# Optimization experiments

Hardware: AMD Instinct MI355X
Metric: run time of the kernel (lower is better)

Reference implementation:

```python
import jax, jax.numpy as jnp
from jax import lax
import numpy as np
import math

D = 96   # d_model
H = 4    # num_heads (d_k = d_v = D per head, per the source)
K = 7    # depthwise kernel size
L = 4    # num conv layers


def _pos_encoding(seq_len, d):
    # Faithful to the source's (nonstandard) exponents: sin uses 2*i/d, cos uses 2*(i+1)/d
    pos = np.arange(seq_len, dtype=np.float32)[:, None]
    i = np.arange(0, d, 2, dtype=np.float32)
    pe = np.zeros((seq_len, d), dtype=np.float32)
    pe[:, 0::2] = np.sin(pos / 10000.0 ** (2.0 * i / d))
    pe[:, 1::2] = np.cos(pos / 10000.0 ** (2.0 * (i + 1.0) / d))
    return jnp.asarray(pe)


def _layernorm(x, g, b, eps=1e-5):
    m = jnp.mean(x, axis=-1, keepdims=True)
    v = jnp.mean((x - m) ** 2, axis=-1, keepdims=True)
    return (x - m) / jnp.sqrt(v + eps) * g + b


def setup_inputs() -> dict:
    key = jax.random.key(0)
    ks = jax.random.split(key, 10)
    B, S = 128, 384

    def xavier(k, shape, fan_in, fan_out):
        bound = math.sqrt(6.0 / (fan_in + fan_out))
        return jax.random.uniform(k, shape, jnp.float32, -bound, bound)

    return {
        "input": jax.random.normal(ks[0], (B, S, D), jnp.float32),
        "mask": jnp.zeros((B, S), dtype=bool),
        "conv_dw": jax.random.normal(ks[1], (L, D, 1, K), jnp.float32) * 0.05,
        "conv_dw_b": jnp.zeros((L, D), jnp.float32),
        "conv_pw": jax.random.normal(ks[2], (L, D, D, 1), jnp.float32) * 0.05,
        "conv_pw_b": jnp.zeros((L, D), jnp.float32),
        "WQ": xavier(ks[3], (H, D, D), D, D),
        "WK": xavier(ks[4], (H, D, D), D, D),
        "WV": xavier(ks[5], (H, D, D), D, D),
        "WO": xavier(ks[6], (H * D, D), H * D, D),
        "ffn_w1": jax.random.normal(ks[7], (D, D // 2), jnp.float32) * 0.1,
        "ffn_b1": jnp.zeros((D // 2,), jnp.float32),
        "ffn_w2": jax.random.normal(ks[8], (D // 2, D), jnp.float32) * 0.1,
        "ffn_b2": jnp.zeros((D,), jnp.float32),
        "ln_g": jnp.ones((L + 2, D), jnp.float32),
        "ln_b": jnp.zeros((L + 2, D), jnp.float32),
    }


def reference(input, mask, conv_dw, conv_dw_b, conv_pw, conv_pw_b,
              WQ, WK, WV, WO, ffn_w1, ffn_b1, ffn_w2, ffn_b2, ln_g, ln_b):
    B, S, _ = input.shape
    dn = ("NCH", "OIH", "NCH")

    # positional encoding (eval mode: all dropout is identity)
    x = input * jnp.float32(math.sqrt(D)) + _pos_encoding(S, D)[None]

    # conv blocks: LN -> depthwise conv -> pointwise conv -> relu -> residual
    for i in range(L):
        h = _layernorm(x, ln_g[i], ln_b[i])
        h = jnp.transpose(h, (0, 2, 1))  # [B, C, S]
        h = lax.conv_general_dilated(h, conv_dw[i], (1,), "SAME",
                                     feature_group_count=D, dimension_numbers=dn)
        h = h + conv_dw_b[i][None, :, None]
        h = lax.conv_general_dilated(h, conv_pw[i], (1,), "SAME", dimension_numbers=dn)
        h = jax.nn.relu(h + conv_pw_b[i][None, :, None])
        x = x + jnp.transpose(h, (0, 2, 1))

    # multi-head attention with per-head full-width projections (d_k = D)
    h = _layernorm(x, ln_g[L], ln_b[L])
    Q = jnp.einsum("bsd,hde->hbse", h, WQ)
    Kh = jnp.einsum("bsd,hde->hbse", h, WK)
    V = jnp.einsum("bsd,hde->hbse", h, WV)
    # source divides scores by temperature = 1/sqrt(d_k) => multiply by sqrt(D)
    scores = jnp.einsum("hbqe,hbke->hbqk", Q, Kh) * jnp.float32(math.sqrt(D))
    # mask is viewed [B, S, 1]: masks query rows, broadcast over keys
    scores = jnp.where(mask[None, :, :, None], -jnp.inf, scores)
    attn = jax.nn.softmax(scores, axis=-1)
    ctx = jnp.einsum("hbqk,hbke->hbqe", attn, V)
    cat = jnp.transpose(ctx, (1, 2, 0, 3)).reshape(B, S, H * D)
    x = x + cat @ WO

    # feed-forward: Linear -> sigmoid -> Linear, residual
    h2 = _layernorm(x, ln_g[L + 1], ln_b[L + 1])
    ff = jax.nn.sigmoid(h2 @ ffn_w1 + ffn_b1) @ ffn_w2 + ffn_b2
    return x + ff
```

## Files before the change

kernel.cpp:

```cpp
#include <hip/hip_runtime.h>
#include <math.h>


constexpr int B = 128;
constexpr int S = 384;
constexpr int D = 96;
constexpr int H = 4;
constexpr int KW = 7;
constexpr int L = 4;
constexpr int ROWS = B * S;
constexpr long long NTOT = (long long)ROWS * D;
constexpr float SQRTD = 9.797958971132712f;

typedef _Float16 f16x8 __attribute__((ext_vector_type(8)));
typedef float f32x4 __attribute__((ext_vector_type(4)));
typedef unsigned short us;
typedef unsigned short us8 __attribute__((ext_vector_type(8)));

__device__ __forceinline__ us f2h(float f) {
    _Float16 h = (_Float16)f;
    return __builtin_bit_cast(us, h);
}
__device__ __forceinline__ f16x8 ldh(const us* p) {
    return *reinterpret_cast<const f16x8*>(p);
}

__global__ void pe_kernel(float* __restrict__ pe) {
    int idx = blockIdx.x * 256 + threadIdx.x;
    if (idx >= S * D) return;
    int s = idx / D, c = idx - s * D;
    int j = c >> 1;
    float expo = (c & 1) ? (4.0f * j + 2.0f) / 96.0f : (4.0f * j) / 96.0f;
    float freq = expf(-expo * logf(10000.0f));
    float ang = (float)s * freq;
    pe[idx] = (c & 1) ? cosf(ang) : sinf(ang);
}

__global__ void prep_w(const float* __restrict__ WQ, const float* __restrict__ WK,
                       const float* __restrict__ cpw, const float* __restrict__ w1,
                       const float* __restrict__ w2,
                       us* __restrict__ wqS, us* __restrict__ wkT, us* __restrict__ pw16,
                       us* __restrict__ w1T, us* __restrict__ w2Tp) {
    int idx = blockIdx.x * 256 + threadIdx.x;
    if (idx >= H * D * D) return;
    int h = idx / (D * D), rem = idx - h * (D * D);
    int d = rem / D, e = rem - d * D;
    int n = e >> 4, lmod = e & 15, kk = d >> 5, ldiv = (d >> 3) & 3, j = d & 7;
    wqS[(size_t)(((h * 6 + n) * 3 + kk) * 64 + ldiv * 16 + lmod) * 8 + j] = f2h(WQ[idx] * SQRTD);
    wkT[(size_t)h * D * D + e * D + d] = f2h(WK[idx]);
    pw16[idx] = f2h(cpw[idx]);
    if (idx < 48 * 96) {
        int m = idx / 96, c = idx - m * 96;
        w1T[idx] = f2h(w1[c * 48 + m]);
    }
    if (idx < 96 * 64) {
        int o = idx / 64, m = idx - o * 64;
        w2Tp[idx] = (m < 48) ? f2h(w2[m * 96 + o]) : (us)0;
    }
}

__global__ void prep_wvo(const float* __restrict__ WV, const float* __restrict__ WO,
                         us* __restrict__ wvoT) {
    int blk = blockIdx.x;
    int h = blk / 6, ot = blk - h * 6;
    int tid = threadIdx.x;
    const float* wv = WV + (size_t)h * D * D;
    const float* wo = WO + (size_t)h * D * D;
    for (int i = tid; i < 16 * 96; i += 256) {
        int o = ot * 16 + i / 96, d = i - (i / 96) * 96;
        float acc = 0.f;
        for (int e = 0; e < 96; e++) acc += wv[d * 96 + e] * wo[e * 96 + o];
        wvoT[(size_t)h * D * D + o * 96 + d] = f2h(acc);
    }
}

__global__ void conv0f(const float* __restrict__ in, const float* __restrict__ pe,
                       const float* __restrict__ g0, const float* __restrict__ b0,
                       float* __restrict__ xout, us* __restrict__ lnout,
                       const float* __restrict__ dwW, const float* __restrict__ dwB,
                       const us* __restrict__ pwW, const float* __restrict__ pwb,
                       const float* __restrict__ gnext, const float* __restrict__ bnext) {
    __shared__ us lnb_s[70 * 104];
    __shared__ us dwb_s[64 * 104];
    __shared__ float lw[96 * 8];
    int tid = threadIdx.x;
    int wave = tid >> 6, lane = tid & 63;
    int r0 = blockIdx.x * 64;
    int b = r0 / S, s0 = r0 % S;

    for (int i = tid; i < 96 * KW; i += 256) lw[(i / KW) * 8 + (i % KW)] = dwW[i];

    for (int i = wave; i < 70; i += 4) {
        int s = s0 - 3 + i;
        bool valid = (unsigned)s < (unsigned)S;
        float v0 = 0.f, v1 = 0.f;
        if (valid) {
            size_t ro = ((size_t)b * S + s) * 96;
            v0 = in[ro + lane] * SQRTD + pe[s * 96 + lane];
            v1 = (lane < 32) ? in[ro + 64 + lane] * SQRTD + pe[s * 96 + 64 + lane] : 0.f;
        }
        float sm = v0 + v1, q = v0 * v0 + v1 * v1;
        for (int off = 32; off > 0; off >>= 1) {
            sm += __shfl_xor(sm, off);
            q += __shfl_xor(q, off);
        }
        float mean = sm * (1.0f / D);
        float var = q * (1.0f / D) - mean * mean;
        float rstd = rsqrtf(var + 1e-5f);
        lnb_s[i * 104 + lane] = f2h(valid ? (v0 - mean) * rstd * g0[lane] + b0[lane] : 0.f);
        if (lane < 32)
            lnb_s[i * 104 + 64 + lane] =
                f2h(valid ? (v1 - mean) * rstd * g0[lane + 64] + b0[lane + 64] : 0.f);
    }
    __syncthreads();

    for (int u = tid; u < 768; u += 256) {
        int j = u / 12, c0 = (u - (u / 12) * 12) * 8;
        float acc[8];
        #pragma unroll
        for (int j2 = 0; j2 < 8; j2++) acc[j2] = dwB[c0 + j2];
        #pragma unroll
        for (int k = 0; k < KW; k++) {
            f16x8 v = ldh(&lnb_s[(j + k) * 104 + c0]);
            #pragma unroll
            for (int j2 = 0; j2 < 8; j2++) acc[j2] += (float)v[j2] * lw[(c0 + j2) * 8 + k];
        }
        us8 o;
        #pragma unroll
        for (int j2 = 0; j2 < 8; j2++) o[j2] = f2h(acc[j2]);
        *reinterpret_cast<us8*>(&dwb_s[j * 104 + c0]) = o;
    }
    __syncthreads();

    int lmod = lane & 15, ldiv = lane >> 4, m0 = wave * 16;
    f32x4 acc[6] = {};
    #pragma unroll
    for (int kk = 0; kk < 3; kk++) {
        f16x8 af = ldh(&dwb_s[(m0 + lmod) * 104 + kk * 32 + ldiv * 8]);
        #pragma unroll
        for (int n = 0; n < 6; n++) {
            f16x8 bf = ldh(pwW + (size_t)(n * 16 + lmod) * 96 + kk * 32 + ldiv * 8);
            acc[n] = __builtin_amdgcn_mfma_f32_16x16x32_f16(af, bf, acc[n], 0, 0, 0);
        }
    }

    float gv[6], bv2[6], pb[6];
    #pragma unroll
    for (int n = 0; n < 6; n++) {
        int o = n * 16 + lmod;
        gv[n] = gnext[o];
        bv2[n] = bnext[o];
        pb[n] = pwb[o];
    }
    #pragma unroll
    for (int n = 0; n < 6; n++) {
        int o = n * 16 + lmod;
        #pragma unroll
        for (int r = 0; r < 4; r++) {
            int sr = m0 + ldiv * 4 + r;
            size_t row = (size_t)r0 + sr;
            float base = in[row * 96 + o] * SQRTD + pe[(s0 + sr) * 96 + o];
            acc[n][r] = base + fmaxf(acc[n][r] + pb[n], 0.f);
        }
    }
    #pragma unroll
    for (int r = 0; r < 4; r++) {
        float sm = 0.f, qq = 0.f;
        #pragma unroll
        for (int n = 0; n < 6; n++) {
            sm += acc[n][r];
            qq += acc[n][r] * acc[n][r];
        }
        #pragma unroll
        for (int st = 1; st <= 8; st <<= 1) {
            sm += __shfl_xor(sm, st);
            qq += __shfl_xor(qq, st);
        }
        float mean = sm * (1.0f / D);
        float var = qq * (1.0f / D) - mean * mean;
        float rstd = rsqrtf(var + 1e-5f);
        size_t row = (size_t)r0 + m0 + ldiv * 4 + r;
        #pragma unroll
        for (int n = 0; n < 6; n++) {
            int o = n * 16 + lmod;
            xout[row * 96 + o] = acc[n][r];
            lnout[row * 96 + o] = f2h((acc[n][r] - mean) * rstd * gv[n] + bv2[n]);
        }
    }
}

__global__ void conv2(const float* __restrict__ xin, const us* __restrict__ lnin,
                      float* __restrict__ xout, us* __restrict__ lnout,
                      const float* __restrict__ dwW, const float* __restrict__ dwB,
                      const us* __restrict__ pwW, const float* __restrict__ pwb,
                      const float* __restrict__ gnext, const float* __restrict__ bnext) {
    __shared__ us dwb_s[64 * 104];
    __shared__ float lw[96 * 8];
    int tid = threadIdx.x;
    int wave = tid >> 6, lane = tid & 63;
    int r0 = blockIdx.x * 64;
    int b = r0 / S, s0 = r0 % S;

    for (int i = tid; i < 96 * KW; i += 256) lw[(i / KW) * 8 + (i % KW)] = dwW[i];
    __syncthreads();

    for (int u = tid; u < 768; u += 256) {
        int j = u / 12, c0 = (u - (u / 12) * 12) * 8;
        float acc[8];
        #pragma unroll
        for (int j2 = 0; j2 < 8; j2++) acc[j2] = dwB[c0 + j2];
        #pragma unroll
        for (int k = 0; k < KW; k++) {
            int ss = s0 + j + k - 3;
            if ((unsigned)ss < (unsigned)S) {
                f16x8 v = ldh(lnin + ((size_t)b * S + ss) * 96 + c0);
                #pragma unroll
                for (int j2 = 0; j2 < 8; j2++) acc[j2] += (float)v[j2] * lw[(c0 + j2) * 8 + k];
            }
        }
        us8 o;
        #pragma unroll
        for (int j2 = 0; j2 < 8; j2++) o[j2] = f2h(acc[j2]);
        *reinterpret_cast<us8*>(&dwb_s[j * 104 + c0]) = o;
    }
    __syncthreads();

    int lmod = lane & 15, ldiv = lane >> 4, m0 = wave * 16;
    f32x4 acc[6] = {};
    #pragma unroll
    for (int kk = 0; kk < 3; kk++) {
        f16x8 af = ldh(&dwb_s[(m0 + lmod) * 104 + kk * 32 + ldiv * 8]);
        #pragma unroll
        for (int n = 0; n < 6; n++) {
            f16x8 bf = ldh(pwW + (size_t)(n * 16 + lmod) * 96 + kk * 32 + ldiv * 8);
            acc[n] = __builtin_amdgcn_mfma_f32_16x16x32_f16(af, bf, acc[n], 0, 0, 0);
        }
    }

    float gv[6], bv2[6], pb[6];
    #pragma unroll
    for (int n = 0; n < 6; n++) {
        int o = n * 16 + lmod;
        gv[n] = gnext[o];
        bv2[n] = bnext[o];
        pb[n] = pwb[o];
    }
    #pragma unroll
    for (int n = 0; n < 6; n++) {
        #pragma unroll
        for (int r = 0; r < 4; r++) {
            size_t row = (size_t)r0 + m0 + ldiv * 4 + r;
            acc[n][r] = xin[row * 96 + n * 16 + lmod] + fmaxf(acc[n][r] + pb[n], 0.f);
        }
    }
    #pragma unroll
    for (int r = 0; r < 4; r++) {
        float sm = 0.f, qq = 0.f;
        #pragma unroll
        for (int n = 0; n < 6; n++) {
            sm += acc[n][r];
            qq += acc[n][r] * acc[n][r];
        }
        #pragma unroll
        for (int st = 1; st <= 8; st <<= 1) {
            sm += __shfl_xor(sm, st);
            qq += __shfl_xor(qq, st);
        }
        float mean = sm * (1.0f / D);
        float var = qq * (1.0f / D) - mean * mean;
        float rstd = rsqrtf(var + 1e-5f);
        size_t row = (size_t)r0 + m0 + ldiv * 4 + r;
        #pragma unroll
        for (int n = 0; n < 6; n++) {
            int o = n * 16 + lmod;
            xout[row * 96 + o] = acc[n][r];
            lnout[row * 96 + o] = f2h((acc[n][r] - mean) * rstd * gv[n] + bv2[n]);
        }
    }
}

__global__ void conv3p(const float* __restrict__ xin, const us* __restrict__ lnin,
                       float* __restrict__ xout, us* __restrict__ lnout,
                       const float* __restrict__ dwW, const float* __restrict__ dwB,
                       const us* __restrict__ pwW, const float* __restrict__ pwb,
                       const float* __restrict__ gnext, const float* __restrict__ bnext,
                       const us* __restrict__ wkT, const us* __restrict__ wvoT,
                       us* __restrict__ Kall, us* __restrict__ Vall) {
    __shared__ float lw[96 * 8];
    __shared__ us stg[96 * 72];
    __shared__ us lnstg[64 * 104];
    int tid = threadIdx.x;
    int wave = tid >> 6, lane = tid & 63;
    int lmod = lane & 15, ldiv = lane >> 4, m0 = wave * 16;
    int r0 = blockIdx.x * 64;
    int b = r0 / S, s0 = r0 % S;

    for (int i = tid; i < 96 * KW; i += 256) lw[(i / KW) * 8 + (i % KW)] = dwW[i];
    __syncthreads();

    for (int u = tid; u < 768; u += 256) {
        int j = u / 12, c0 = (u - (u / 12) * 12) * 8;
        float acc[8];
        #pragma unroll
        for (int j2 = 0; j2 < 8; j2++) acc[j2] = dwB[c0 + j2];
        #pragma unroll
        for (int k = 0; k < KW; k++) {
            int ss = s0 + j + k - 3;
            if ((unsigned)ss < (unsigned)S) {
                f16x8 v = ldh(lnin + ((size_t)b * S + ss) * 96 + c0);
                #pragma unroll
                for (int j2 = 0; j2 < 8; j2++) acc[j2] += (float)v[j2] * lw[(c0 + j2) * 8 + k];
            }
        }
        us8 o;
        #pragma unroll
        for (int j2 = 0; j2 < 8; j2++) o[j2] = f2h(acc[j2]);
        *reinterpret_cast<us8*>(&stg[j * 104 + c0]) = o;
    }
    __syncthreads();

    f32x4 acc[6] = {};
    #pragma unroll
    for (int kk = 0; kk < 3; kk++) {
        f16x8 af = ldh(&stg[(m0 + lmod) * 104 + kk * 32 + ldiv * 8]);
        #pragma unroll
        for (int n = 0; n < 6; n++) {
            f16x8 bf = ldh(pwW + (size_t)(n * 16 + lmod) * 96 + kk * 32 + ldiv * 8);
            acc[n] = __builtin_amdgcn_mfma_f32_16x16x32_f16(af, bf, acc[n], 0, 0, 0);
        }
    }

    float gv[6], bv2[6], pb[6];
    #pragma unroll
    for (int n = 0; n < 6; n++) {
        int o = n * 16 + lmod;
        gv[n] = gnext[o];
        bv2[n] = bnext[o];
        pb[n] = pwb[o];
    }
    #pragma unroll
    for (int n = 0; n < 6; n++) {
        #pragma unroll
        for (int r = 0; r < 4; r++) {
            size_t row = (size_t)r0 + m0 + ldiv * 4 + r;
            acc[n][r] = xin[row * 96 + n * 16 + lmod] + fmaxf(acc[n][r] + pb[n], 0.f);
        }
    }
    #pragma unroll
    for (int r = 0; r < 4; r++) {
        float sm = 0.f, qq = 0.f;
        #pragma unroll
        for (int n = 0; n < 6; n++) {
            sm += acc[n][r];
            qq += acc[n][r] * acc[n][r];
        }
        #pragma unroll
        for (int st = 1; st <= 8; st <<= 1) {
            sm += __shfl_xor(sm, st);
            qq += __shfl_xor(qq, st);
        }
        float mean = sm * (1.0f / D);
        float var = qq * (1.0f / D) - mean * mean;
        float rstd = rsqrtf(var + 1e-5f);
        size_t row = (size_t)r0 + m0 + ldiv * 4 + r;
        #pragma unroll
        for (int n = 0; n < 6; n++) {
            int o = n * 16 + lmod;
            xout[row * 96 + o] = acc[n][r];
            us hv = f2h((acc[n][r] - mean) * rstd * gv[n] + bv2[n]);
            lnout[row * 96 + o] = hv;
            lnstg[(m0 + ldiv * 4 + r) * 104 + o] = hv;
        }
    }
    __syncthreads();

    f16x8 af[3];
    #pragma unroll
    for (int kk = 0; kk < 3; kk++)
        af[kk] = ldh(&lnstg[(m0 + lmod) * 104 + kk * 32 + ldiv * 8]);

    for (int hd = 0; hd < H; hd++) {
        f32x4 ka[6] = {};
        #pragma unroll
        for (int kk = 0; kk < 3; kk++)
            #pragma unroll
            for (int n = 0; n < 6; n++) {
                f16x8 bf =
                    ldh(wkT + (size_t)hd * D * D + (size_t)(n * 16 + lmod) * 96 + kk * 32 + ldiv * 8);
                ka[n] = __builtin_amdgcn_mfma_f32_16x16x32_f16(af[kk], bf, ka[n], 0, 0, 0);
            }
        __syncthreads();
        us* kT = stg + wave * 1664;
        #pragma unroll
        for (int n = 0; n < 6; n++)
            #pragma unroll
            for (int r = 0; r < 4; r++)
                kT[(ldiv * 4 + r) * 104 + n * 16 + lmod] = f2h(ka[n][r]);
        int t0 = (r0 % S) / 16 + wave;
        us* dst = Kall + (size_t)hd * NTOT + ((size_t)(b * 24 + t0) * 3) * 512;
        #pragma unroll
        for (int kk = 0; kk < 3; kk++) {
            us8 v = *reinterpret_cast<const us8*>(&kT[lmod * 104 + kk * 32 + ldiv * 8]);
            *reinterpret_cast<us8*>(dst + kk * 512 + lane * 8) = v;
        }
        f32x4 va[6] = {};
        #pragma unroll
        for (int kk = 0; kk < 3; kk++)
            #pragma unroll
            for (int n = 0; n < 6; n++) {
                f16x8 bf = ldh(wvoT + (size_t)hd * D * D + (size_t)(n * 16 + lmod) * 96 + kk * 32 +
                               ldiv * 8);
                va[n] = __builtin_amdgcn_mfma_f32_16x16x32_f16(af[kk], bf, va[n], 0, 0, 0);
            }
        __syncthreads();
        #pragma unroll
        for (int n = 0; n < 6; n++)
            #pragma unroll
            for (int r = 0; r < 4; r++)
                stg[(n * 16 + lmod) * 72 + m0 + ldiv * 4 + r] = f2h(va[n][r]);
        __syncthreads();
        int cblk = (r0 % S) / 64;
        us* dsth = Vall + (size_t)hd * NTOT;
        #pragma unroll
        for (int n = 0; n < 6; n++)
            #pragma unroll
            for (int kk = 0; kk < 2; kk++) {
                us8 v =
                    *reinterpret_cast<const us8*>(&stg[(n * 16 + lmod) * 72 + kk * 32 + ldiv * 8]);
                *reinterpret_cast<us8*>(
                    dsth + ((size_t)((b * 6 + n) * 6 + cblk) * 2 + kk) * 512 + lane * 8) = v;
            }
    }
}

__global__ __launch_bounds__(256, 2) void attn_2p4(const us* __restrict__ h16,
                                                   const us* __restrict__ wqS,
                                                   const us* __restrict__ Kall,
                                                   const us* __restrict__ Vall,
                                                   us* __restrict__ xpart) {
    __shared__ us stg4[4][32 * 104];
    int tid = threadIdx.x, wave = tid >> 6, lane = tid & 63;
    us* stg = stg4[wave];
    int lmod = lane & 15, ldiv = lane >> 4;
    int p = blockIdx.x;
    int gl = (((p & 7) * 192 + (p >> 3)) << 2) + wave;
    int t = gl % 12;
    int bh = gl / 12;
    int b = bh >> 2, hd = bh & 3;
    size_t rowbase = (size_t)b * S + t * 32;

    f16x8 ah0[3], ah1[3];
    #pragma unroll
    for (int kk = 0; kk < 3; kk++) {
        ah0[kk] = ldh(h16 + (rowbase + lmod) * 96 + kk * 32 + ldiv * 8);
        ah1[kk] = ldh(h16 + (rowbase + 16 + lmod) * 96 + kk * 32 + ldiv * 8);
    }

    f32x4 qa0[6] = {}, qa1[6] = {};
    #pragma unroll
    for (int kk = 0; kk < 3; kk++)
        #pragma unroll
        for (int n = 0; n < 6; n++) {
            f16x8 bf = ldh(wqS + (size_t)(((hd * 6 + n) * 3 + kk) * 64) * 8 + lane * 8);
            qa0[n] = __builtin_amdgcn_mfma_f32_16x16x32_f16(ah0[kk], bf, qa0[n], 0, 0, 0);
            qa1[n] = __builtin_amdgcn_mfma_f32_16x16x32_f16(ah1[kk], bf, qa1[n], 0, 0, 0);
        }
    #pragma unroll
    for (int n = 0; n < 6; n++)
        #pragma unroll
        for (int r = 0; r < 4; r++) {
            stg[(ldiv * 4 + r) * 104 + n * 16 + lmod] = f2h(qa0[n][r]);
            stg[(16 + ldiv * 4 + r) * 104 + n * 16 + lmod] = f2h(qa1[n][r]);
        }
    f16x8 aq0[3], aq1[3];
    #pragma unroll
    for (int kk = 0; kk < 3; kk++) {
        aq0[kk] = ldh(&stg[lmod * 104 + kk * 32 + ldiv * 8]);
        aq1[kk] = ldh(&stg[(16 + lmod) * 104 + kk * 32 + ldiv * 8]);
    }

    const us* Kh = Kall + (size_t)hd * NTOT + (size_t)b * 24 * 1536;
    const us* Vh = Vall + (size_t)hd * NTOT + (size_t)b * 36 * 1024;

    f32x4 mx0 = {-1e30f, -1e30f, -1e30f, -1e30f}, mx1 = mx0;
    for (int c = 0; c < 6; c++) {
        f32x4 s0[4] = {}, s1[4] = {};
        __builtin_amdgcn_s_setprio(1);
        #pragma unroll
        for (int nt = 0; nt < 4; nt++)
            #pragma unroll
            for (int kk = 0; kk < 3; kk++) {
                f16x8 bf = ldh(Kh + (size_t)((c * 4 + nt) * 3 + kk) * 512 + lane * 8);
                s0[nt] = __builtin_amdgcn_mfma_f32_16x16x32_f16(aq0[kk], bf, s0[nt], 0, 0, 0);
                s1[nt] = __builtin_amdgcn_mfma_f32_16x16x32_f16(aq1[kk], bf, s1[nt], 0, 0, 0);
            }
        __builtin_amdgcn_s_setprio(0);
        #pragma unroll
        for (int nt = 0; nt < 4; nt++)
            #pragma unroll
            for (int r = 0; r < 4; r++) {
                mx0[r] = fmaxf(mx0[r], s0[nt][r]);
                mx1[r] = fmaxf(mx1[r], s1[nt][r]);
            }
    }
    #pragma unroll
    for (int st = 1; st <= 8; st <<= 1)
        #pragma unroll
        for (int r = 0; r < 4; r++) {
            mx0[r] = fmaxf(mx0[r], __shfl_xor(mx0[r], st));
            mx1[r] = fmaxf(mx1[r], __shfl_xor(mx1[r], st));
        }

    f32x4 oacc0[6] = {}, oacc1[6] = {};
    f32x4 l0v = {}, l1v = {};
    for (int c = 0; c < 6; c++) {
        f32x4 s0[4] = {}, s1[4] = {};
        __builtin_amdgcn_s_setprio(1);
        #pragma unroll
        for (int nt = 0; nt < 4; nt++)
            #pragma unroll
            for (int kk = 0; kk < 3; kk++) {
                f16x8 bf = ldh(Kh + (size_t)((c * 4 + nt) * 3 + kk) * 512 + lane * 8);
                s0[nt] = __builtin_amdgcn_mfma_f32_16x16x32_f16(aq0[kk], bf, s0[nt], 0, 0, 0);
                s1[nt] = __builtin_amdgcn_mfma_f32_16x16x32_f16(aq1[kk], bf, s1[nt], 0, 0, 0);
            }
        __builtin_amdgcn_s_setprio(0);
        #pragma unroll
        for (int nt = 0; nt < 4; nt++)
            #pragma unroll
            for (int r = 0; r < 4; r++) {
                float p0 = __expf(s0[nt][r] - mx0[r]);
                float p1 = __expf(s1[nt][r] - mx1[r]);
                l0v[r] += p0;
                l1v[r] += p1;
                stg[(ldiv * 4 + r) * 72 + nt * 16 + lmod] = f2h(p0);
                stg[(16 + ldiv * 4 + r) * 72 + nt * 16 + lmod] = f2h(p1);
            }
        __builtin_amdgcn_s_setprio(1);
        #pragma unroll
        for (int kk = 0; kk < 2; kk++) {
            f16x8 pf0 = ldh(&stg[lmod * 72 + kk * 32 + ldiv * 8]);
            f16x8 pf1 = ldh(&stg[(16 + lmod) * 72 + kk * 32 + ldiv * 8]);
            #pragma unroll
            for (int n = 0; n < 6; n++) {
                f16x8 bf = ldh(Vh + (size_t)((n * 6 + c) * 2 + kk) * 512 + lane * 8);
                oacc0[n] = __builtin_amdgcn_mfma_f32_16x16x32_f16(pf0, bf, oacc0[n], 0, 0, 0);
                oacc1[n] = __builtin_amdgcn_mfma_f32_16x16x32_f16(pf1, bf, oacc1[n], 0, 0, 0);
            }
        }
        __builtin_amdgcn_s_setprio(0);
    }
    #pragma unroll
    for (int st = 1; st <= 8; st <<= 1)
        #pragma unroll
        for (int r = 0; r < 4; r++) {
            l0v[r] += __shfl_xor(l0v[r], st);
            l1v[r] += __shfl_xor(l1v[r], st);
        }

    us* xp = xpart + (size_t)hd * NTOT;
    #pragma unroll
    for (int r = 0; r < 4; r++) {
        float inv0 = 1.f / l0v[r];
        float inv1 = 1.f / l1v[r];
        #pragma unroll
        for (int n = 0; n < 6; n++) {
            xp[(rowbase + ldiv * 4 + r) * 96 + n * 16 + lmod] = f2h(oacc0[n][r] * inv0);
            xp[(rowbase + 16 + ldiv * 4 + r) * 96 + n * 16 + lmod] = f2h(oacc1[n][r] * inv1);
        }
    }
}

__global__ void ffn_ln(const float* __restrict__ x, const us* __restrict__ xpart,
                       const float* __restrict__ gln, const float* __restrict__ bln,
                       const us* __restrict__ w1T, const float* __restrict__ b1,
                       const us* __restrict__ w2Tp, const float* __restrict__ b2,
                       float* __restrict__ out) {
    __shared__ float xf[64 * 96];
    __shared__ us lnb[64 * 104];
    __shared__ us mid[64 * 72];
    int tid = threadIdx.x, wave = tid >> 6, lane = tid & 63;
    int lmod = lane & 15, ldiv = lane >> 4, m0 = wave * 16;
    int row0 = blockIdx.x * 64;

    for (int i = wave; i < 64; i += 4) {
        size_t ro = (size_t)(row0 + i) * 96;
        float v0 = x[ro + lane];
        float v1 = (lane < 32) ? x[ro + 64 + lane] : 0.f;
        #pragma unroll
        for (int h = 0; h < H; h++) {
            const us* xp = xpart + (size_t)h * NTOT + ro;
            v0 += (float)__builtin_bit_cast(_Float16, xp[lane]);
            if (lane < 32) v1 += (float)__builtin_bit_cast(_Float16, xp[64 + lane]);
        }
        xf[i * 96 + lane] = v0;
        if (lane < 32) xf[i * 96 + 64 + lane] = v1;
        float sm = v0 + v1, q = v0 * v0 + v1 * v1;
        for (int off = 32; off > 0; off >>= 1) {
            sm += __shfl_xor(sm, off);
            q += __shfl_xor(q, off);
        }
        float mean = sm * (1.0f / D);
        float var = q * (1.0f / D) - mean * mean;
        float rstd = rsqrtf(var + 1e-5f);
        lnb[i * 104 + lane] = f2h((v0 - mean) * rstd * gln[lane] + bln[lane]);
        if (lane < 32)
            lnb[i * 104 + 64 + lane] = f2h((v1 - mean) * rstd * gln[lane + 64] + bln[lane + 64]);
    }
    __syncthreads();

    f32x4 a3[3] = {};
    #pragma unroll
    for (int kk = 0; kk < 3; kk++) {
        f16x8 af = ldh(&lnb[(m0 + lmod) * 104 + kk * 32 + ldiv * 8]);
        #pragma unroll
        for (int n = 0; n < 3; n++) {
            f16x8 bf = ldh(w1T + (size_t)(n * 16 + lmod) * 96 + kk * 32 + ldiv * 8);
            a3[n] = __builtin_amdgcn_mfma_f32_16x16x32_f16(af, bf, a3[n], 0, 0, 0);
        }
    }
    #pragma unroll
    for (int n = 0; n < 3; n++) {
        float bv = b1[n * 16 + lmod];
        #pragma unroll
        for (int r = 0; r < 4; r++) {
            float v = a3[n][r] + bv;
            mid[(m0 + ldiv * 4 + r) * 72 + n * 16 + lmod] = f2h(1.f / (1.f + __expf(-v)));
        }
    }
    #pragma unroll
    for (int r = 0; r < 4; r++) mid[(m0 + ldiv * 4 + r) * 72 + 48 + lmod] = 0;
    __syncthreads();

    f32x4 a6[6] = {};
    #pragma unroll
    for (int kk = 0; kk < 2; kk++) {
        f16x8 af = ldh(&mid[(m0 + lmod) * 72 + kk * 32 + ldiv * 8]);
        #pragma unroll
        for (int n = 0; n < 6; n++) {
            f16x8 bf = ldh(w2Tp + (size_t)(n * 16 + lmod) * 64 + kk * 32 + ldiv * 8);
            a6[n] = __builtin_amdgcn_mfma_f32_16x16x32_f16(af, bf, a6[n], 0, 0, 0);
        }
    }
    #pragma unroll
    for (int n = 0; n < 6; n++) {
        int o = n * 16 + lmod;
        float bv = b2[o];
        #pragma unroll
        for (int r = 0; r < 4; r++) {
            int sr = m0 + ldiv * 4 + r;
            out[(size_t)(row0 + sr) * 96 + o] = xf[sr * 96 + o] + a6[n][r] + bv;
        }
    }
}

extern "C" void kernel_launch(void* const* d_in, const int* in_sizes, int n_in,
                              void* d_out, int out_size, void* d_ws, size_t ws_size,
                              hipStream_t stream) {
    const float* in   = (const float*)d_in[0];
    const float* cdw  = (const float*)d_in[2];
    const float* cdwb = (const float*)d_in[3];
    const float* cpw  = (const float*)d_in[4];
    const float* cpwb = (const float*)d_in[5];
    const float* WQ   = (const float*)d_in[6];
    const float* WK   = (const float*)d_in[7];
    const float* WV   = (const float*)d_in[8];
    const float* WO   = (const float*)d_in[9];
    const float* w1   = (const float*)d_in[10];
    const float* b1   = (const float*)d_in[11];
    const float* w2   = (const float*)d_in[12];
    const float* b2   = (const float*)d_in[13];
    const float* lng  = (const float*)d_in[14];
    const float* lnb  = (const float*)d_in[15];
    float* out = (float*)d_out;
    float* ws = (float*)d_ws;

    float* xA  = ws;
    float* xB  = xA + NTOT;
    float* pe  = xB + NTOT;
    us* lnA    = (us*)(pe + S * D);
    us* lnB    = lnA + NTOT;
    us* Kall   = lnB + NTOT;
    us* Vall   = Kall + (size_t)H * NTOT;
    us* xpart  = Vall + (size_t)H * NTOT;
    us* wqS    = xpart + (size_t)H * NTOT;
    us* wkT    = wqS + H * D * D;
    us* wvoT   = wkT + H * D * D;
    us* pw16   = wvoT + H * D * D;
    us* w1T    = pw16 + L * D * D;
    us* w2Tp   = w1T + 48 * 96;

    pe_kernel<<<(S * D + 255) / 256, 256, 0, stream>>>(pe);
    prep_w<<<(H * D * D + 255) / 256, 256, 0, stream>>>(WQ, WK, cpw, w1, w2,
                                                        wqS, wkT, pw16, w1T, w2Tp);
    prep_wvo<<<H * 6, 256, 0, stream>>>(WV, WO, wvoT);

    conv0f<<<ROWS / 64, 256, 0, stream>>>(in, pe, lng, lnb, xA, lnB,
                                          cdw, cdwb, pw16, cpwb, lng + D, lnb + D);
    conv2<<<ROWS / 64, 256, 0, stream>>>(xA, lnB, xB, lnA, cdw + D * KW, cdwb + D,
                                         pw16 + D * D, cpwb + D, lng + 2 * D, lnb + 2 * D);
    conv2<<<ROWS / 64, 256, 0, stream>>>(xB, lnA, xA, lnB, cdw + 2 * D * KW, cdwb + 2 * D,
                                         pw16 + 2 * D * D, cpwb + 2 * D, lng + 3 * D,
                                         lnb + 3 * D);
    conv3p<<<ROWS / 64, 256, 0, stream>>>(xA, lnB, xB, lnA, cdw + 3 * D * KW, cdwb + 3 * D,
                                          pw16 + 3 * D * D, cpwb + 3 * D, lng + 4 * D,
                                          lnb + 4 * D, wkT, wvoT, Kall, Vall);

    attn_2p4<<<1536, 256, 0, stream>>>(lnA, wqS, Kall, Vall, xpart);

    ffn_ln<<<ROWS / 64, 256, 0, stream>>>(xB, xpart, lng + 5 * D, lnb + 5 * D,
                                          w1T, b1, w2Tp, b2, out);
}
```

Baseline: 334.4 us.

## Software-pipeline attention second pass with double-buffered P tiles

Restructures the softmax/PV loop so the QK scores for chunk c+1 are computed before the PV MFMAs for chunk c, with the exponentiated probabilities written to alternating LDS buffers. The aim is to overlap score MFMAs and global K loads with PV work and the exp/store phase, hiding latency within each wave. It adds extra LDS per block (a second P buffer) and raises register pressure from holding two score sets live, which could cause spills under the two-blocks-per-CU launch bound.

Result: no change. 337.8 us (+1.0%).

```diff
diff --git a/kernel.cpp b/kernel.cpp
--- a/kernel.cpp
+++ b/kernel.cpp
@@ -433,14 +433,52 @@
     }
 }
 
+#define SCORE(CC, S0, S1)                                                                   \
+    __builtin_amdgcn_s_setprio(1);                                                          \
+    _Pragma("unroll") for (int nt = 0; nt < 4; nt++) {                                      \
+        _Pragma("unroll") for (int kk = 0; kk < 3; kk++) {                                  \
+            f16x8 bf = ldh(Kh + (size_t)(((CC) * 4 + nt) * 3 + kk) * 512 + lane * 8);       \
+            S0[nt] = __builtin_amdgcn_mfma_f32_16x16x32_f16(aq0[kk], bf, S0[nt], 0, 0, 0);  \
+            S1[nt] = __builtin_amdgcn_mfma_f32_16x16x32_f16(aq1[kk], bf, S1[nt], 0, 0, 0);  \
+        }                                                                                   \
+    }                                                                                       \
+    __builtin_amdgcn_s_setprio(0);
+
+#define EXPSTORE(S0, S1, BUF)                                      \
+    _Pragma("unroll") for (int nt = 0; nt < 4; nt++) {             \
+        _Pragma("unroll") for (int r = 0; r < 4; r++) {            \
+            float p0 = __expf(S0[nt][r] - mx0[r]);                 \
+            float p1 = __expf(S1[nt][r] - mx1[r]);                 \
+            l0v[r] += p0;                                          \
+            l1v[r] += p1;                                          \
+            (BUF)[(ldiv * 4 + r) * 72 + nt * 16 + lmod] = f2h(p0); \
+            (BUF)[(16 + ldiv * 4 + r) * 72 + nt * 16 + lmod] = f2h(p1); \
+        }                                                          \
+    }
+
+#define PVSTEP(CC, BUF)                                                                     \
+    __builtin_amdgcn_s_setprio(1);                                                          \
+    _Pragma("unroll") for (int kk = 0; kk < 2; kk++) {                                      \
+        f16x8 pf0 = ldh((BUF) + lmod * 72 + kk * 32 + ldiv * 8);                            \
+        f16x8 pf1 = ldh((BUF) + (16 + lmod) * 72 + kk * 32 + ldiv * 8);                     \
+        _Pragma("unroll") for (int n = 0; n < 6; n++) {                                     \
+            f16x8 bf = ldh(Vh + (size_t)((n * 6 + (CC)) * 2 + kk) * 512 + lane * 8);        \
+            oacc0[n] = __builtin_amdgcn_mfma_f32_16x16x32_f16(pf0, bf, oacc0[n], 0, 0, 0);  \
+            oacc1[n] = __builtin_amdgcn_mfma_f32_16x16x32_f16(pf1, bf, oacc1[n], 0, 0, 0);  \
+        }                                                                                   \
+    }                                                                                       \
+    __builtin_amdgcn_s_setprio(0);
+
 __global__ __launch_bounds__(256, 2) void attn_2p4(const us* __restrict__ h16,
                                                    const us* __restrict__ wqS,
                                                    const us* __restrict__ Kall,
                                                    const us* __restrict__ Vall,
                                                    us* __restrict__ xpart) {
     __shared__ us stg4[4][32 * 104];
+    __shared__ us stgP[4][32 * 72];
     int tid = threadIdx.x, wave = tid >> 6, lane = tid & 63;
     us* stg = stg4[wave];
+    us* bufB = stgP[wave];
     int lmod = lane & 15, ldiv = lane >> 4;
     int p = blockIdx.x;
     int gl = (((p & 7) * 192 + (p >> 3)) << 2) + wave;
@@ -485,16 +523,7 @@
     f32x4 mx0 = {-1e30f, -1e30f, -1e30f, -1e30f}, mx1 = mx0;
     for (int c = 0; c < 6; c++) {
         f32x4 s0[4] = {}, s1[4] = {};
-        __builtin_amdgcn_s_setprio(1);
-        #pragma unroll
-        for (int nt = 0; nt < 4; nt++)
-            #pragma unroll
-            for (int kk = 0; kk < 3; kk++) {
-                f16x8 bf = ldh(Kh + (size_t)((c * 4 + nt) * 3 + kk) * 512 + lane * 8);
-                s0[nt] = __builtin_amdgcn_mfma_f32_16x16x32_f16(aq0[kk], bf, s0[nt], 0, 0, 0);
-                s1[nt] = __builtin_amdgcn_mfma_f32_16x16x32_f16(aq1[kk], bf, s1[nt], 0, 0, 0);
-            }
-        __builtin_amdgcn_s_setprio(0);
+        SCORE(c, s0, s1)
         #pragma unroll
         for (int nt = 0; nt < 4; nt++)
             #pragma unroll
@@ -513,42 +542,22 @@
 
     f32x4 oacc0[6] = {}, oacc1[6] = {};
     f32x4 l0v = {}, l1v = {};
+    {
+        f32x4 s0[4] = {}, s1[4] = {};
+        SCORE(0, s0, s1)
+        EXPSTORE(s0, s1, stg)
+    }
     for (int c = 0; c < 6; c++) {
-        f32x4 s0[4] = {}, s1[4] = {};
-        __builtin_amdgcn_s_setprio(1);
-        #pragma unroll
-        for (int nt = 0; nt < 4; nt++)
-            #pragma unroll
-            for (int kk = 0; kk < 3; kk++) {
-                f16x8 bf = ldh(Kh + (size_t)((c * 4 + nt) * 3 + kk) * 512 + lane * 8);
-                s0[nt] = __builtin_amdgcn_mfma_f32_16x16x32_f16(aq0[kk], bf, s0[nt], 0, 0, 0);
-                s1[nt] = __builtin_amdgcn_mfma_f32_16x16x32_f16(aq1[kk], bf, s1[nt], 0, 0, 0);
-            }
-        __builtin_amdgcn_s_setprio(0);
-        #pragma unroll
-        for (int nt = 0; nt < 4; nt++)
-            #pragma unroll
-            for (int r = 0; r < 4; r++) {
-                float p0 = __expf(s0[nt][r] - mx0[r]);
-                float p1 = __expf(s1[nt][r] - mx1[r]);
-                l0v[r] += p0;
-                l1v[r] += p1;
-                stg[(ldiv * 4 + r) * 72 + nt * 16 + lmod] = f2h(p0);
-                stg[(16 + ldiv * 4 + r) * 72 + nt * 16 + lmod] = f2h(p1);
-            }
-        __builtin_amdgcn_s_setprio(1);
-        #pragma unroll
-        for (int kk = 0; kk < 2; kk++) {
-            f16x8 pf0 = ldh(&stg[lmod * 72 + kk * 32 + ldiv * 8]);
-            f16x8 pf1 = ldh(&stg[(16 + lmod) * 72 + kk * 32 + ldiv * 8]);
-            #pragma unroll
-            for (int n = 0; n < 6; n++) {
-                f16x8 bf = ldh(Vh + (size_t)((n * 6 + c) * 2 + kk) * 512 + lane * 8);
-                oacc0[n] = __builtin_amdgcn_mfma_f32_16x16x32_f16(pf0, bf, oacc0[n], 0, 0, 0);
-                oacc1[n] = __builtin_amdgcn_mfma_f32_16x16x32_f16(pf1, bf, oacc1[n], 0, 0, 0);
-            }
-        }
-        __builtin_amdgcn_s_setprio(0);
+        f32x4 t0[4] = {}, t1[4] = {};
+        if (c < 5) {
+            SCORE(c + 1, t0, t1)
+        }
+        us* rb = (c & 1) ? bufB : stg;
+        PVSTEP(c, rb)
+        if (c < 5) {
+            us* wb = (c & 1) ? stg : bufB;
+            EXPSTORE(t0, t1, wb)
+        }
     }
     #pragma unroll
     for (int st = 1; st <= 8; st <<= 1)
```

## Share K/V tiles across waves via double-buffered LDS in attention kernel

Applied to the files above, without the earlier changes.

The attention kernel is restructured so that each block's four waves handle 128 consecutive queries of the same batch/head and cooperatively stage K and V chunks into double-buffered shared memory. Previously each wave streamed K and V from global memory on its own. The V tensor layout written by the conv3p kernel is reordered so that each key chunk is contiguous. This cuts redundant global/L2 traffic for K/V, at the cost of block-wide barriers each chunk and roughly 75KB of LDS per block, which may limit the intended two blocks per CU.

Result: faster. 304.5 us (-8.9%).

```diff
diff --git a/kernel.cpp b/kernel.cpp
--- a/kernel.cpp
+++ b/kernel.cpp
@@ -428,69 +428,91 @@
                 us8 v =
                     *reinterpret_cast<const us8*>(&stg[(n * 16 + lmod) * 72 + kk * 32 + ldiv * 8]);
                 *reinterpret_cast<us8*>(
-                    dsth + ((size_t)((b * 6 + n) * 6 + cblk) * 2 + kk) * 512 + lane * 8) = v;
-            }
-    }
-}
-
-__global__ __launch_bounds__(256, 2) void attn_2p4(const us* __restrict__ h16,
-                                                   const us* __restrict__ wqS,
-                                                   const us* __restrict__ Kall,
-                                                   const us* __restrict__ Vall,
-                                                   us* __restrict__ xpart) {
-    __shared__ us stg4[4][32 * 104];
+                    dsth + ((size_t)((b * 6 + cblk) * 6 + n) * 2 + kk) * 512 + lane * 8) = v;
+            }
+    }
+}
+
+__global__ __launch_bounds__(256, 2) void attn_g(const us* __restrict__ h16,
+                                                 const us* __restrict__ wqS,
+                                                 const us* __restrict__ Kall,
+                                                 const us* __restrict__ Vall,
+                                                 us* __restrict__ xpart) {
+    __shared__ us Kb[2][6144];
+    __shared__ us Vb[2][6144];
+    __shared__ us Pq[4][3328];
     int tid = threadIdx.x, wave = tid >> 6, lane = tid & 63;
-    us* stg = stg4[wave];
     int lmod = lane & 15, ldiv = lane >> 4;
     int p = blockIdx.x;
-    int gl = (((p & 7) * 192 + (p >> 3)) << 2) + wave;
-    int t = gl % 12;
-    int bh = gl / 12;
+    int gl = (p & 7) * 192 + (p >> 3);
+    int qt = gl % 3;
+    int bh = gl / 3;
     int b = bh >> 2, hd = bh & 3;
-    size_t rowbase = (size_t)b * S + t * 32;
-
-    f16x8 ah0[3], ah1[3];
-    #pragma unroll
-    for (int kk = 0; kk < 3; kk++) {
-        ah0[kk] = ldh(h16 + (rowbase + lmod) * 96 + kk * 32 + ldiv * 8);
-        ah1[kk] = ldh(h16 + (rowbase + 16 + lmod) * 96 + kk * 32 + ldiv * 8);
-    }
-
-    f32x4 qa0[6] = {}, qa1[6] = {};
-    #pragma unroll
-    for (int kk = 0; kk < 3; kk++)
-        #pragma unroll
-        for (int n = 0; n < 6; n++) {
-            f16x8 bf = ldh(wqS + (size_t)(((hd * 6 + n) * 3 + kk) * 64) * 8 + lane * 8);
-            qa0[n] = __builtin_amdgcn_mfma_f32_16x16x32_f16(ah0[kk], bf, qa0[n], 0, 0, 0);
-            qa1[n] = __builtin_amdgcn_mfma_f32_16x16x32_f16(ah1[kk], bf, qa1[n], 0, 0, 0);
-        }
-    #pragma unroll
-    for (int n = 0; n < 6; n++)
-        #pragma unroll
-        for (int r = 0; r < 4; r++) {
-            stg[(ldiv * 4 + r) * 104 + n * 16 + lmod] = f2h(qa0[n][r]);
-            stg[(16 + ldiv * 4 + r) * 104 + n * 16 + lmod] = f2h(qa1[n][r]);
-        }
-    f16x8 aq0[3], aq1[3];
-    #pragma unroll
-    for (int kk = 0; kk < 3; kk++) {
-        aq0[kk] = ldh(&stg[lmod * 104 + kk * 32 + ldiv * 8]);
-        aq1[kk] = ldh(&stg[(16 + lmod) * 104 + kk * 32 + ldiv * 8]);
-    }
+    size_t rowbase = (size_t)b * S + qt * 128 + wave * 32;
 
     const us* Kh = Kall + (size_t)hd * NTOT + (size_t)b * 24 * 1536;
     const us* Vh = Vall + (size_t)hd * NTOT + (size_t)b * 36 * 1024;
+    us* P = Pq[wave];
+
+    us8 kst[3];
+    #pragma unroll
+    for (int j = 0; j < 3; j++)
+        kst[j] = *reinterpret_cast<const us8*>(Kh + (size_t)(j * 256 + tid) * 8);
+
+    f32x4 qa0[6] = {}, qa1[6] = {};
+    #pragma unroll
+    for (int kk = 0; kk < 3; kk++) {
+        f16x8 a0 = ldh(h16 + (rowbase + lmod) * 96 + kk * 32 + ldiv * 8);
+        f16x8 a1 = ldh(h16 + (rowbase + 16 + lmod) * 96 + kk * 32 + ldiv * 8);
+        #pragma unroll
+        for (int n = 0; n < 6; n++) {
+            f16x8 bf = ldh(wqS + (size_t)(((hd * 6 + n) * 3 + kk) * 64) * 8 + lane * 8);
+            qa0[n] = __builtin_amdgcn_mfma_f32_16x16x32_f16(a0, bf, qa0[n], 0, 0, 0);
+            qa1[n] = __builtin_amdgcn_mfma_f32_16x16x32_f16(a1, bf, qa1[n], 0, 0, 0);
+        }
+    }
+    #pragma unroll
+    for (int n = 0; n < 6; n++)
+        #pragma unroll
+        for (int r = 0; r < 4; r++) {
+            P[(ldiv * 4 + r) * 104 + n * 16 + lmod] = f2h(qa0[n][r]);
+            P[(16 + ldiv * 4 + r) * 104 + n * 16 + lmod] = f2h(qa1[n][r]);
+        }
+    f16x8 aq0[3], aq1[3];
+    #pragma unroll
+    for (int kk = 0; kk < 3; kk++) {
+        aq0[kk] = ldh(&P[lmod * 104 + kk * 32 + ldiv * 8]);
+        aq1[kk] = ldh(&P[(16 + lmod) * 104 + kk * 32 + ldiv * 8]);
+    }
+    #pragma unroll
+    for (int j = 0; j < 3; j++)
+        *reinterpret_cast<us8*>(&Kb[0][(j * 256 + tid) * 8]) = kst[j];
+    __syncthreads();
 
     f32x4 mx0 = {-1e30f, -1e30f, -1e30f, -1e30f}, mx1 = mx0;
     for (int c = 0; c < 6; c++) {
+        int cur = c & 1, nxt = cur ^ 1;
+        us8 kn[3], vn[3];
+        bool last = (c == 5);
+        if (!last) {
+            #pragma unroll
+            for (int j = 0; j < 3; j++)
+                kn[j] = *reinterpret_cast<const us8*>(Kh + (size_t)(c + 1) * 6144 +
+                                                      (size_t)(j * 256 + tid) * 8);
+        } else {
+            #pragma unroll
+            for (int j = 0; j < 3; j++) {
+                kn[j] = *reinterpret_cast<const us8*>(Kh + (size_t)(j * 256 + tid) * 8);
+                vn[j] = *reinterpret_cast<const us8*>(Vh + (size_t)(j * 256 + tid) * 8);
+            }
+        }
+        __builtin_amdgcn_s_setprio(1);
         f32x4 s0[4] = {}, s1[4] = {};
-        __builtin_amdgcn_s_setprio(1);
         #pragma unroll
         for (int nt = 0; nt < 4; nt++)
             #pragma unroll
             for (int kk = 0; kk < 3; kk++) {
-                f16x8 bf = ldh(Kh + (size_t)((c * 4 + nt) * 3 + kk) * 512 + lane * 8);
+                f16x8 bf = ldh(&Kb[cur][(nt * 3 + kk) * 512 + lane * 8]);
                 s0[nt] = __builtin_amdgcn_mfma_f32_16x16x32_f16(aq0[kk], bf, s0[nt], 0, 0, 0);
                 s1[nt] = __builtin_amdgcn_mfma_f32_16x16x32_f16(aq1[kk], bf, s1[nt], 0, 0, 0);
             }
@@ -502,6 +524,16 @@
                 mx0[r] = fmaxf(mx0[r], s0[nt][r]);
                 mx1[r] = fmaxf(mx1[r], s1[nt][r]);
             }
+        int wb = last ? 0 : nxt;
+        #pragma unroll
+        for (int j = 0; j < 3; j++)
+            *reinterpret_cast<us8*>(&Kb[wb][(j * 256 + tid) * 8]) = kn[j];
+        if (last) {
+            #pragma unroll
+            for (int j = 0; j < 3; j++)
+                *reinterpret_cast<us8*>(&Vb[0][(j * 256 + tid) * 8]) = vn[j];
+        }
+        __syncthreads();
     }
     #pragma unroll
     for (int st = 1; st <= 8; st <<= 1)
@@ -514,13 +546,24 @@
     f32x4 oacc0[6] = {}, oacc1[6] = {};
     f32x4 l0v = {}, l1v = {};
     for (int c = 0; c < 6; c++) {
+        int cur = c & 1, nxt = cur ^ 1;
+        us8 kn[3], vn[3];
+        if (c < 5) {
+            #pragma unroll
+            for (int j = 0; j < 3; j++) {
+                kn[j] = *reinterpret_cast<const us8*>(Kh + (size_t)(c + 1) * 6144 +
+                                                      (size_t)(j * 256 + tid) * 8);
+                vn[j] = *reinterpret_cast<const us8*>(Vh + (size_t)(c + 1) * 6144 +
+                                                      (size_t)(j * 256 + tid) * 8);
+            }
+        }
+        __builtin_amdgcn_s_setprio(1);
         f32x4 s0[4] = {}, s1[4] = {};
-        __builtin_amdgcn_s_setprio(1);
         #pragma unroll
         for (int nt = 0; nt < 4; nt++)
             #pragma unroll
             for (int kk = 0; kk < 3; kk++) {
-                f16x8 bf = ldh(Kh + (size_t)((c * 4 + nt) * 3 + kk) * 512 + lane * 8);
+                f16x8 bf = ldh(&Kb[cur][(nt * 3 + kk) * 512 + lane * 8]);
                 s0[nt] = __builtin_amdgcn_mfma_f32_16x16x32_f16(aq0[kk], bf, s0[nt], 0, 0, 0);
                 s1[nt] = __builtin_amdgcn_mfma_f32_16x16x32_f16(aq1[kk], bf, s1[nt], 0, 0, 0);
             }
@@ -533,22 +576,30 @@
                 float p1 = __expf(s1[nt][r] - mx1[r]);
                 l0v[r] += p0;
                 l1v[r] += p1;
-                stg[(ldiv * 4 + r) * 72 + nt * 16 + lmod] = f2h(p0);
-                stg[(16 + ldiv * 4 + r) * 72 + nt * 16 + lmod] = f2h(p1);
+                P[(ldiv * 4 + r) * 72 + nt * 16 + lmod] = f2h(p0);
+                P[(16 + ldiv * 4 + r) * 72 + nt * 16 + lmod] = f2h(p1);
             }
         __builtin_amdgcn_s_setprio(1);
         #pragma unroll
         for (int kk = 0; kk < 2; kk++) {
-            f16x8 pf0 = ldh(&stg[lmod * 72 + kk * 32 + ldiv * 8]);
-            f16x8 pf1 = ldh(&stg[(16 + lmod) * 72 + kk * 32 + ldiv * 8]);
+            f16x8 pf0 = ldh(&P[lmod * 72 + kk * 32 + ldiv * 8]);
+            f16x8 pf1 = ldh(&P[(16 + lmod) * 72 + kk * 32 + ldiv * 8]);
             #pragma unroll
             for (int n = 0; n < 6; n++) {
-                f16x8 bf = ldh(Vh + (size_t)((n * 6 + c) * 2 + kk) * 512 + lane * 8);
+                f16x8 bf = ldh(&Vb[cur][(n * 2 + kk) * 512 + lane * 8]);
                 oacc0[n] = __builtin_amdgcn_mfma_f32_16x16x32_f16(pf0, bf, oacc0[n], 0, 0, 0);
                 oacc1[n] = __builtin_amdgcn_mfma_f32_16x16x32_f16(pf1, bf, oacc1[n], 0, 0, 0);
             }
         }
         __builtin_amdgcn_s_setprio(0);
+        if (c < 5) {
+            #pragma unroll
+            for (int j = 0; j < 3; j++) {
+                *reinterpret_cast<us8*>(&Kb[nxt][(j * 256 + tid) * 8]) = kn[j];
+                *reinterpret_cast<us8*>(&Vb[nxt][(j * 256 + tid) * 8]) = vn[j];
+            }
+            __syncthreads();
+        }
     }
     #pragma unroll
     for (int st = 1; st <= 8; st <<= 1)
@@ -706,7 +757,7 @@
                                           pw16 + 3 * D * D, cpwb + 3 * D, lng + 4 * D,
                                           lnb + 4 * D, wkT, wvoT, Kall, Vall);
 
-    attn_2p4<<<1536, 256, 0, stream>>>(lnA, wqS, Kall, Vall, xpart);
+    attn_g<<<1536, 256, 0, stream>>>(lnA, wqS, Kall, Vall, xpart);
 
     ffn_ln<<<ROWS / 64, 256, 0, stream>>>(xB, xpart, lng + 5 * D, lnb + 5 * D,
                                           w1T, b1, w2Tp, b2, out);
```
